# Kernel tuning notes

Hardware: AMD Instinct MI355X
Metric: run time of the kernel (lower is better)

The kernel has to match this reference:

```python
import jax, jax.numpy as jnp
import numpy as np

N_NODES = 100000
N_EDGES = 400000
F_IN = 128
HEADS = 4
C1 = 64   # conv1 out per head
C2 = 128  # conv2 out per head
G = 2048  # num graphs
FP = 2048
HID = 64
NEG_SLOPE = 0.2


def _gat_conv(x, edge_index, W, a_src, a_dst, b, heads, ch):
    """PyG-style GATConv with self-loops, concat=True."""
    n = x.shape[0]
    loops = jnp.arange(n, dtype=edge_index.dtype)
    src = jnp.concatenate([edge_index[0], loops])
    dst = jnp.concatenate([edge_index[1], loops])
    h = (x @ W).reshape(n, heads, ch)                      # [N,H,C]
    e_src = jnp.sum(h * a_src, axis=-1)                    # [N,H]
    e_dst = jnp.sum(h * a_dst, axis=-1)                    # [N,H]
    logits = jax.nn.leaky_relu(e_src[src] + e_dst[dst], NEG_SLOPE)  # [E,H]
    m = jax.ops.segment_max(logits, dst, num_segments=n)   # per-dst max
    p = jnp.exp(logits - m[dst])
    denom = jax.ops.segment_sum(p, dst, num_segments=n)
    alpha = p / denom[dst]                                 # [E,H]
    out = jax.ops.segment_sum(h[src] * alpha[:, :, None], dst, num_segments=n)
    return out.reshape(n, heads * ch) + b


def setup_inputs() -> dict:
    key = jax.random.key(0)
    ks = jax.random.split(key, 16)
    s = 0.05
    inp = {
        "x": jax.random.normal(ks[0], (N_NODES, F_IN), jnp.float32),
        "edge_index": jax.random.randint(ks[1], (2, N_EDGES), 0, N_NODES, jnp.int32),
        "batch": jnp.sort(jax.random.randint(ks[2], (N_NODES,), 0, G, jnp.int32)),
        "fp": jax.random.normal(ks[3], (G, FP), jnp.float32),
        "W1": jax.random.normal(ks[4], (F_IN, HEADS * C1), jnp.float32) * s,
        "a_src1": jax.random.normal(ks[5], (HEADS, C1), jnp.float32) * s,
        "a_dst1": jax.random.normal(ks[6], (HEADS, C1), jnp.float32) * s,
        "b1": jnp.zeros((HEADS * C1,), jnp.float32),
        "W2": jax.random.normal(ks[7], (HEADS * C1, HEADS * C2), jnp.float32) * s,
        "a_src2": jax.random.normal(ks[8], (HEADS, C2), jnp.float32) * s,
        "a_dst2": jax.random.normal(ks[9], (HEADS, C2), jnp.float32) * s,
        "b2": jnp.zeros((HEADS * C2,), jnp.float32),
        "Wfp": jax.random.normal(ks[10], (FP, HID), jnp.float32) * s,
        "bfp": jnp.zeros((HID,), jnp.float32),
        "Wfc1": jax.random.normal(ks[11], (HEADS * C2 + HID, HID), jnp.float32) * s,
        "bfc1": jnp.zeros((HID,), jnp.float32),
        "Wfc2": jax.random.normal(ks[12], (HID, 1), jnp.float32) * s,
        "bfc2": jnp.zeros((1,), jnp.float32),
    }
    return inp


def reference(x, edge_index, batch, fp, W1, a_src1, a_dst1, b1, W2, a_src2, a_dst2, b2,
              Wfp, bfp, Wfc1, bfc1, Wfc2, bfc2):
    h = _gat_conv(x, edge_index, W1, a_src1, a_dst1, b1, HEADS, C1)
    h = jax.nn.elu(h)
    h = _gat_conv(h, edge_index, W2, a_src2, a_dst2, b2, HEADS, C2)
    h = jax.nn.elu(h)
    # global mean pool over graphs
    sums = jax.ops.segment_sum(h, batch, num_segments=G)
    counts = jax.ops.segment_sum(jnp.ones((h.shape[0], 1), h.dtype), batch, num_segments=G)
    pooled = sums / jnp.maximum(counts, 1.0)               # [G, 512]
    fph = fp @ Wfp + bfp                                   # [G, 64]
    z = jnp.concatenate([pooled, fph], axis=1)             # [G, 576]
    z = jax.nn.relu(z @ Wfc1 + bfc1)
    # dropout is identity in eval mode
    return z @ Wfc2 + bfc2                                 # [G, 1]
```

## Files before the change

### kernel.cpp

```cpp
#include <hip/hip_runtime.h>
#include <math.h>

#define NEG_SLOPE 0.2f

typedef __attribute__((ext_vector_type(8))) short bf16x8;
typedef __attribute__((ext_vector_type(4))) float f32x4;
typedef __attribute__((ext_vector_type(2))) float f32x2;

__device__ __forceinline__ float b2f(short s) {
  return __uint_as_float(((unsigned int)(unsigned short)s) << 16);
}
__device__ __forceinline__ unsigned short f2b_rne(float f) {
  unsigned int u = __float_as_uint(f);
  u = (u + 0x7FFF + ((u >> 16) & 1)) >> 16;
  return (unsigned short)u;
}

__device__ __forceinline__ void fp8x8_to_f32(uint2 raw, float* f) {
  f32x2 a = __builtin_amdgcn_cvt_pk_f32_fp8((int)raw.x, false);
  f32x2 b = __builtin_amdgcn_cvt_pk_f32_fp8((int)raw.x, true);
  f32x2 c = __builtin_amdgcn_cvt_pk_f32_fp8((int)raw.y, false);
  f32x2 d = __builtin_amdgcn_cvt_pk_f32_fp8((int)raw.y, true);
  f[0] = a[0]; f[1] = a[1]; f[2] = b[0]; f[3] = b[1];
  f[4] = c[0]; f[5] = c[1]; f[6] = d[0]; f[7] = d[1];
}

__device__ __forceinline__ void gload16(const unsigned short* g, unsigned short* l) {
  __builtin_amdgcn_global_load_lds(
      (const __attribute__((address_space(1))) unsigned int*)g,
      (__attribute__((address_space(3))) unsigned int*)l, 16, 0, 0);
}

template<int N> __device__ __forceinline__ void vmwait() {
  asm volatile("s_waitcnt vmcnt(%0)" :: "n"(N) : "memory");
}

__device__ __forceinline__ unsigned int bsel(uint4 d, int s) {
  return ((d.x >> (8 * s)) & 0xffu) | (((d.y >> (8 * s)) & 0xffu) << 8)
       | (((d.z >> (8 * s)) & 0xffu) << 16) | (((d.w >> (8 * s)) & 0xffu) << 24);
}

__device__ __forceinline__ void tr_one(const float* __restrict__ W,
                                       unsigned short* __restrict__ WT,
                                       int K, int N, int idx)
{
  if (idx < K * N) {
    int k = idx / N, n = idx - k * N;
    WT[(size_t)n * K + k] = f2b_rne(W[idx]);
  }
}

__global__ __launch_bounds__(256) void prep_all(
    const float* __restrict__ x, unsigned short* __restrict__ xb, size_t nx, int B0,
    const float* __restrict__ fp, unsigned short* __restrict__ fpb, size_t nf, int B1,
    const float* __restrict__ W1, unsigned short* __restrict__ W1T,
    const float* __restrict__ W2, unsigned short* __restrict__ W2T,
    const float* __restrict__ Wfp, unsigned short* __restrict__ WfpT,
    const float* __restrict__ Wfc1, unsigned short* __restrict__ Wfc1T)
{
  int b = blockIdx.x;
  const int t = threadIdx.x;
  if (b < B0) {
    size_t i = (size_t)b * 256 + t;
    if (i < nx) xb[i] = f2b_rne(x[i]);
    return;
  }
  b -= B0;
  if (b < B1) {
    size_t i = (size_t)b * 256 + t;
    if (i < nf) fpb[i] = f2b_rne(fp[i]);
    return;
  }
  b -= B1;
  if (b < 128) { tr_one(W1, W1T, 128, 256, b * 256 + t); return; }
  b -= 128;
  if (b < 512) { tr_one(W2, W2T, 256, 512, b * 256 + t); return; }
  b -= 512;
  if (b < 512) { tr_one(Wfp, WfpT, 2048, 64, b * 256 + t); return; }
  b -= 512;
  tr_one(Wfc1, Wfc1T, 576, 64, b * 256 + t);
}

__global__ __launch_bounds__(256) void prep_e(
    const float* __restrict__ W1, const float* __restrict__ as1, const float* __restrict__ ad1,
    const float* __restrict__ W2, const float* __restrict__ as2, const float* __restrict__ ad2,
    unsigned short* __restrict__ BeT1, unsigned short* __restrict__ BeT2)
{
  const int b = blockIdx.x;
  const int k = threadIdx.x;
  if (b < 4) {
    if (k < 128) {
      float ss = 0.f, sd = 0.f;
      for (int c = 0; c < 64; ++c) {
        float w = W1[k * 256 + b * 64 + c];
        ss += w * as1[b * 64 + c];
        sd += w * ad1[b * 64 + c];
      }
      BeT1[b * 128 + k] = f2b_rne(ss);
      BeT1[(4 + b) * 128 + k] = f2b_rne(sd);
    }
  } else {
    const int h = b - 4;
    float ss = 0.f, sd = 0.f;
    for (int c = 0; c < 128; ++c) {
      float w = W2[k * 512 + h * 128 + c];
      ss += w * as2[h * 128 + c];
      sd += w * ad2[h * 128 + c];
    }
    BeT2[h * 256 + k] = f2b_rne(ss);
    BeT2[(4 + h) * 256 + k] = f2b_rne(sd);
  }
}

template<int KK>
__global__ __launch_bounds__(256) void gemm_mfma(
    const unsigned short* __restrict__ A, const unsigned short* __restrict__ BT,
    unsigned char* __restrict__ Cout, int M, int N,
    const unsigned short* __restrict__ BeT,
    float* __restrict__ es, float* __restrict__ ed, int nh)
{
  constexpr int NT = KK / 32;
  constexpr int LDE = KK + 8;
  __shared__ unsigned short As[4][128 * 32];
  __shared__ unsigned short Bs[4][128 * 32];
  __shared__ unsigned short Be[16 * LDE];
  const int tid  = threadIdx.x;
  const int wave = tid >> 6;
  const int lane = tid & 63;
  const int ln   = lane & 15;
  const int quad = lane >> 4;
  const int wr0  = (wave >> 1) * 64;
  const int wc0  = (wave & 1) * 64;

  const int nwg = gridDim.x;
  const int ncol = N >> 7;
  const int bid = blockIdx.x;
  const int qq = nwg >> 3, rr = nwg & 7;
  const int xc = bid & 7, io = bid >> 3;
  const int swz = (xc < rr ? xc * (qq + 1) : rr * (qq + 1) + (xc - rr) * qq) + io;
  const int bn = (swz % ncol) * 128;
  const int bm = (swz / ncol) * 128;
  const bool do_e = (bn == 0) && (wc0 == 0);

  if (bn == 0 && tid < KK) {
    const int rrw = tid / (KK / 8);
    const int ccl = (tid % (KK / 8)) * 8;
    bf16x8 v = *(const bf16x8*)(BeT + rrw * KK + ccl);
    *(bf16x8*)(&Be[rrw * LDE + ccl]) = v;
  }
  __syncthreads();

  const int srow = lane >> 2;
  const int cch  = lane & 3;
  const int rt0  = wave * 32 + srow;
  const int ksw  = ((cch ^ (srow & 3)) << 3);
  int ar0 = bm + rt0;      if (ar0 >= M) ar0 = M - 1;
  int ar1 = bm + rt0 + 16; if (ar1 >= M) ar1 = M - 1;
  const unsigned short* gA0 = A + (size_t)ar0 * KK + ksw;
  const unsigned short* gA1 = A + (size_t)ar1 * KK + ksw;
  const unsigned short* gB0 = BT + (size_t)(bn + rt0) * KK + ksw;
  const unsigned short* gB1 = BT + (size_t)(bn + rt0 + 16) * KK + ksw;

  auto stage = [&](int T) {
    const int b = T & 3;
    const int kk = T * 32;
    gload16(gA0 + kk, &As[b][(wave * 32) * 32]);
    gload16(gA1 + kk, &As[b][(wave * 32 + 16) * 32]);
    gload16(gB0 + kk, &Bs[b][(wave * 32) * 32]);
    gload16(gB1 + kk, &Bs[b][(wave * 32 + 16) * 32]);
  };

  f32x4 acc[4][4];
  f32x4 acc_e[4];
  const f32x4 z4 = {0.f, 0.f, 0.f, 0.f};
#pragma unroll
  for (int i = 0; i < 4; ++i) {
    acc_e[i] = z4;
#pragma unroll
    for (int j = 0; j < 4; ++j) acc[i][j] = z4;
  }

  stage(0); stage(1); stage(2);

#pragma unroll
  for (int t = 0; t < NT; ++t) {
    if (t + 3 < NT) stage(t + 3);
    if      (t < NT - 3) vmwait<12>();
    else if (t == NT - 3) vmwait<8>();
    else if (t == NT - 2) vmwait<4>();
    else                  vmwait<0>();
    __builtin_amdgcn_s_barrier();
    __builtin_amdgcn_sched_barrier(0);
    const int b = t & 3;
    bf16x8 af[4], bfv[4];
#pragma unroll
    for (int i = 0; i < 4; ++i) {
      const int row = wr0 + i * 16 + ln;
      af[i] = *(const bf16x8*)(&As[b][row * 32 + ((quad ^ (ln & 3)) << 3)]);
    }
#pragma unroll
    for (int j = 0; j < 4; ++j) {
      const int row = wc0 + j * 16 + ln;
      bfv[j] = *(const bf16x8*)(&Bs[b][row * 32 + ((quad ^ (ln & 3)) << 3)]);
    }
#pragma unroll
    for (int i = 0; i < 4; ++i)
#pragma unroll
      for (int j = 0; j < 4; ++j)
        acc[i][j] = __builtin_amdgcn_mfma_f32_16x16x32_bf16(af[i], bfv[j], acc[i][j], 0, 0, 0);
    if (do_e) {
      bf16x8 bfe = *(const bf16x8*)(&Be[ln * LDE + t * 32 + quad * 8]);
#pragma unroll
      for (int i = 0; i < 4; ++i)
        acc_e[i] = __builtin_amdgcn_mfma_f32_16x16x32_bf16(af[i], bfe, acc_e[i], 0, 0, 0);
    }
    __builtin_amdgcn_sched_barrier(0);
    __builtin_amdgcn_s_barrier();
  }
  __syncthreads();

  unsigned int* Cb = (unsigned int*)As;
  const int cbase = (wc0 >> 2) + ln;
#pragma unroll
  for (int i = 0; i < 4; ++i) {
#pragma unroll
    for (int r = 0; r < 4; ++r) {
      int rowl = wr0 + i * 16 + quad * 4 + r;
      int p = __builtin_amdgcn_cvt_pk_fp8_f32(acc[i][0][r], acc[i][1][r], 0, false);
      p     = __builtin_amdgcn_cvt_pk_fp8_f32(acc[i][2][r], acc[i][3][r], p, true);
      Cb[rowl * 36 + cbase] = (unsigned int)p;
    }
  }
  if (do_e) {
#pragma unroll
    for (int i = 0; i < 4; ++i) {
#pragma unroll
      for (int r = 0; r < 4; ++r) {
        int row = bm + wr0 + i * 16 + quad * 4 + r;
        if (row < M && ln < 8) {
          float* dst = (ln < 4) ? es : ed;
          dst[(size_t)row * nh + (ln & 3)] = acc_e[i][r];
        }
      }
    }
  }
  __syncthreads();

  {
    const int rT = tid >> 1;
    const int hT = tid & 1;
    const unsigned int* cp = &Cb[rT * 36 + 16 * hT];
    uint4 d0 = *(const uint4*)(cp + 0);
    uint4 d1 = *(const uint4*)(cp + 4);
    uint4 d2 = *(const uint4*)(cp + 8);
    uint4 d3 = *(const uint4*)(cp + 12);
    int grow = bm + rT;
    if (grow < M) {
      unsigned char* gp = Cout + (size_t)grow * N + bn + 64 * hT;
      uint4 o;
      o.x = bsel(d0, 0); o.y = bsel(d1, 0); o.z = bsel(d2, 0); o.w = bsel(d3, 0);
      *(uint4*)(gp + 0) = o;
      o.x = bsel(d0, 1); o.y = bsel(d1, 1); o.z = bsel(d2, 1); o.w = bsel(d3, 1);
      *(uint4*)(gp + 16) = o;
      o.x = bsel(d0, 2); o.y = bsel(d1, 2); o.z = bsel(d2, 2); o.w = bsel(d3, 2);
      *(uint4*)(gp + 32) = o;
      o.x = bsel(d0, 3); o.y = bsel(d1, 3); o.z = bsel(d2, 3); o.w = bsel(d3, 3);
      *(uint4*)(gp + 48) = o;
    }
  }
}

__global__ __launch_bounds__(256) void gemm_mfma_n64(
    const unsigned short* __restrict__ A, int lda,
    const unsigned short* __restrict__ BT, int ldb,
    float* __restrict__ Cp, int M, int kchunk)
{
  const int LDT = 72;
  __shared__ unsigned short As[128 * 72];
  __shared__ unsigned short Bs[64 * 72];
  const int tid  = threadIdx.x;
  const int wave = tid >> 6;
  const int lane = tid & 63;
  const int ln   = lane & 15;
  const int quad = lane >> 4;
  const int ks   = blockIdx.x;
  const int bm   = blockIdx.y * 128;
  const int k_beg = ks * kchunk;
  const int k_end = k_beg + kchunk;
  const int arow = tid >> 1;
  const int akb  = (tid & 1) * 32;
  const int brow = tid >> 2;
  const int bkb  = (tid & 3) * 16;

  f32x4 acc[2][4];
  const f32x4 z4 = {0.f, 0.f, 0.f, 0.f};
#pragma unroll
  for (int i = 0; i < 2; ++i)
#pragma unroll
    for (int j = 0; j < 4; ++j) acc[i][j] = z4;

  for (int k0 = k_beg; k0 < k_end; k0 += 64) {
    const unsigned short* ap = A + (size_t)(bm + arow) * lda + k0 + akb;
#pragma unroll
    for (int q = 0; q < 4; ++q)
      *(bf16x8*)(&As[arow * LDT + akb + q * 8]) = *(const bf16x8*)(ap + q * 8);
    const unsigned short* bp = BT + (size_t)brow * ldb + k0 + bkb;
#pragma unroll
    for (int q = 0; q < 2; ++q)
      *(bf16x8*)(&Bs[brow * LDT + bkb + q * 8]) = *(const bf16x8*)(bp + q * 8);
    __syncthreads();
#pragma unroll
    for (int kk = 0; kk < 2; ++kk) {
      bf16x8 af[2], bfv[4];
#pragma unroll
      for (int i = 0; i < 2; ++i)
        af[i] = *(const bf16x8*)(&As[(wave * 32 + i * 16 + ln) * LDT + kk * 32 + quad * 8]);
#pragma unroll
      for (int j = 0; j < 4; ++j)
        bfv[j] = *(const bf16x8*)(&Bs[(j * 16 + ln) * LDT + kk * 32 + quad * 8]);
#pragma unroll
      for (int i = 0; i < 2; ++i)
#pragma unroll
        for (int j = 0; j < 4; ++j)
          acc[i][j] = __builtin_amdgcn_mfma_f32_16x16x32_bf16(af[i], bfv[j], acc[i][j], 0, 0, 0);
    }
    __syncthreads();
  }
#pragma unroll
  for (int i = 0; i < 2; ++i)
#pragma unroll
    for (int r = 0; r < 4; ++r) {
      int row = bm + wave * 32 + i * 16 + quad * 4 + r;
#pragma unroll
      for (int j = 0; j < 4; ++j)
        Cp[((size_t)ks * M + row) * 64 + j * 16 + ln] = acc[i][j][r];
    }
}

__global__ void fp_finish(const float* __restrict__ Cp, int ksplit, int M,
                          const float* __restrict__ bfp,
                          unsigned short* __restrict__ zb)
{
  const int g = blockIdx.x;
  const int j = threadIdx.x;
  float s = bfp[j];
  for (int ks = 0; ks < ksplit; ++ks) s += Cp[((size_t)ks * M + g) * 64 + j];
  zb[(size_t)g * 576 + 512 + j] = f2b_rne(s);
}

__global__ void mlp_finish(const float* __restrict__ Cp, int ksplit, int M,
                           const float* __restrict__ bfc1,
                           const float* __restrict__ Wfc2, const float* __restrict__ bfc2,
                           float* __restrict__ out)
{
  const int g = blockIdx.x;
  const int j = threadIdx.x;
  float s = bfc1[j];
  for (int ks = 0; ks < ksplit; ++ks) s += Cp[((size_t)ks * M + g) * 64 + j];
  s = s > 0.f ? s : 0.f;
  float term = s * Wfc2[j];
  for (int off = 32; off; off >>= 1) term += __shfl_down(term, off, 64);
  if (j == 0) out[g] = term + bfc2[0];
}

__global__ void count_all(const int* __restrict__ ei, int E, int* __restrict__ deg,
                          const int* __restrict__ batch, int NN, int* __restrict__ gcnt,
                          int BE)
{
  int b = blockIdx.x;
  int t = threadIdx.x;
  if (b < BE) {
    int e = b * 256 + t;
    if (e < E) atomicAdd(&deg[ei[E + e]], 1);
  } else {
    int i = (b - BE) * 256 + t;
    if (i < NN) atomicAdd(&gcnt[batch[i]], 1);
  }
}

__global__ void fill_csr(const int* __restrict__ ei, int E, int* __restrict__ cursor,
                         const int* __restrict__ rowptr, int* __restrict__ csr_src)
{
  int e = blockIdx.x * 256 + threadIdx.x;
  if (e < E) {
    int d = ei[E + e];
    int pos = atomicAdd(&cursor[d], 1);
    csr_src[rowptr[d] + pos] = ei[e];
  }
}

__device__ void scan_p1_body(const int* __restrict__ vals, int n, int* __restrict__ bsum,
                             int bb)
{
  __shared__ int red[256];
  int base = bb * 1024;
  int t = threadIdx.x;
  int s = 0;
#pragma unroll
  for (int i = 0; i < 4; ++i) {
    int idx = base + i * 256 + t;
    if (idx < n) s += vals[idx];
  }
  red[t] = s;
  __syncthreads();
  for (int off = 128; off; off >>= 1) {
    if (t < off) red[t] += red[t + off];
    __syncthreads();
  }
  if (t == 0) bsum[bb] = red[0];
}

__global__ void scan2_p1(const int* __restrict__ vA, int nA, int* __restrict__ bsA, int nbA,
                         const int* __restrict__ vB, int nB, int* __restrict__ bsB)
{
  int b = blockIdx.x;
  if (b < nbA) scan_p1_body(vA, nA, bsA, b);
  else         scan_p1_body(vB, nB, bsB, b - nbA);
}

__device__ void scan_p2_body(const int* __restrict__ bsum, int* __restrict__ bpre,
                             int nb, int* __restrict__ rowptr, int n)
{
  __shared__ int tmp[128];
  int t = threadIdx.x;
  int v = (t < nb) ? bsum[t] : 0;
  tmp[t] = v;
  __syncthreads();
  for (int off = 1; off < 128; off <<= 1) {
    int add = (t >= off) ? tmp[t - off] : 0;
    __syncthreads();
    tmp[t] += add;
    __syncthreads();
  }
  if (t < nb) bpre[t] = tmp[t] - v;
  if (t == 127) rowptr[n] = tmp[127];
}

__global__ void scan2_p2(const int* __restrict__ bsA, int* __restrict__ bpA, int nbA,
                         int* __restrict__ rpA, int nA,
                         const int* __restrict__ bsB, int* __restrict__ bpB, int nbB,
                         int* __restrict__ rpB, int nB)
{
  if (blockIdx.x == 0) scan_p2_body(bsA, bpA, nbA, rpA, nA);
  else                 scan_p2_body(bsB, bpB, nbB, rpB, nB);
}

__device__ void scan_p3_body(const int* __restrict__ vals, const int* __restrict__ bpre,
                             int n, int* __restrict__ rowptr, int bb)
{
  __shared__ int tmp[256];
  int t = threadIdx.x;
  int base = bb * 1024 + t * 4;
  int v[4]; int s = 0;
#pragma unroll
  for (int i = 0; i < 4; ++i) {
    int idx = base + i;
    v[i] = (idx < n) ? vals[idx] : 0;
    s += v[i];
  }
  tmp[t] = s;
  __syncthreads();
  for (int off = 1; off < 256; off <<= 1) {
    int add = (t >= off) ? tmp[t - off] : 0;
    __syncthreads();
    tmp[t] += add;
    __syncthreads();
  }
  int run = bpre[bb] + tmp[t] - s;
#pragma unroll
  for (int i = 0; i < 4; ++i) {
    int idx = base + i;
    if (idx < n) rowptr[idx] = run;
    run += v[i];
  }
}

__global__ void scan2_p3(const int* __restrict__ vA, const int* __restrict__ bpA, int nA,
                         int* __restrict__ rpA, int nbA,
                         const int* __restrict__ vB, const int* __restrict__ bpB, int nB,
                         int* __restrict__ rpB)
{
  int b = blockIdx.x;
  if (b < nbA) scan_p3_body(vA, bpA, nA, rpA, b);
  else         scan_p3_body(vB, bpB, nB, rpB, b - nbA);
}

__global__ void alpha_kernel(const float* __restrict__ es, const float* __restrict__ ed,
                             const int* __restrict__ rowptr, const int* __restrict__ csr_src,
                             float* __restrict__ w_csr, float* __restrict__ wself,
                             float* __restrict__ dinv, int N, int nh)
{
  int idx = blockIdx.x * 256 + threadIdx.x;
  if (idx >= N * nh) return;
  const int dst = idx / nh;
  const int h = idx - dst * nh;
  const float edh = ed[(size_t)dst * nh + h];
  const int beg = rowptr[dst], end = rowptr[dst + 1];
  float sum = 0.f;
  for (int e = beg; e < end; ++e) {
    int s = csr_src[e];
    float l = es[(size_t)s * nh + h] + edh;
    l = l >= 0.f ? l : NEG_SLOPE * l;
    float w = expf(l);
    w_csr[(size_t)e * nh + h] = w;
    sum += w;
  }
  float ls = es[(size_t)dst * nh + h] + edh;
  ls = ls >= 0.f ? ls : NEG_SLOPE * ls;
  float wsl = expf(ls);
  sum += wsl;
  wself[(size_t)dst * nh + h] = wsl;
  dinv[(size_t)dst * nh + h] = 1.0f / sum;
}

__global__ __launch_bounds__(256) void aggregate_b(
    const unsigned char* __restrict__ h,
    const float* __restrict__ w_csr, const float* __restrict__ wself,
    const float* __restrict__ dinv,
    const int* __restrict__ rowptr, const int* __restrict__ csr_src,
    const float* __restrict__ bias, unsigned short* __restrict__ out,
    int N, int nh, int C)
{
  const int HC = nh * C;
  const int CH8 = HC >> 3;
  const int dpb = 256 / CH8;
  const int grp = threadIdx.x / CH8;
  const int lane = threadIdx.x - grp * CH8;
  const int dst = blockIdx.x * dpb + grp;
  if (dst >= N) return;
  const int ch = lane << 3;
  const int head = ch / C;
  const int beg = rowptr[dst], end = rowptr[dst + 1];
  float acc[8] = {0.f, 0.f, 0.f, 0.f, 0.f, 0.f, 0.f, 0.f};
  float hv[8];
  int e = beg;
  for (; e + 1 < end; e += 2) {
    int s0 = csr_src[e], s1 = csr_src[e + 1];
    float a0 = w_csr[(size_t)e * nh + head];
    float a1 = w_csr[(size_t)(e + 1) * nh + head];
    uint2 r0 = *(const uint2*)(h + (size_t)s0 * HC + ch);
    uint2 r1 = *(const uint2*)(h + (size_t)s1 * HC + ch);
    fp8x8_to_f32(r0, hv);
#pragma unroll
    for (int r = 0; r < 8; ++r) acc[r] = fmaf(a0, hv[r], acc[r]);
    fp8x8_to_f32(r1, hv);
#pragma unroll
    for (int r = 0; r < 8; ++r) acc[r] = fmaf(a1, hv[r], acc[r]);
  }
  if (e < end) {
    int s0 = csr_src[e];
    float a0 = w_csr[(size_t)e * nh + head];
    uint2 r0 = *(const uint2*)(h + (size_t)s0 * HC + ch);
    fp8x8_to_f32(r0, hv);
#pragma unroll
    for (int r = 0; r < 8; ++r) acc[r] = fmaf(a0, hv[r], acc[r]);
  }
  {
    float a = wself[(size_t)dst * nh + head];
    uint2 r0 = *(const uint2*)(h + (size_t)dst * HC + ch);
    fp8x8_to_f32(r0, hv);
#pragma unroll
    for (int r = 0; r < 8; ++r) acc[r] = fmaf(a, hv[r], acc[r]);
  }
  const float di = dinv[(size_t)dst * nh + head];
  bf16x8 o;
#pragma unroll
  for (int r = 0; r < 8; ++r) {
    float v = acc[r] * di + bias[ch + r];
    v = v > 0.f ? v : (expf(v) - 1.0f);
    o[r] = (short)f2b_rne(v);
  }
  *(bf16x8*)(out + (size_t)dst * HC + ch) = o;
}

__global__ __launch_bounds__(256) void agg_pool(
    const unsigned char* __restrict__ h,
    const float* __restrict__ w_csr, const float* __restrict__ wself,
    const float* __restrict__ dinv,
    const int* __restrict__ rowptr, const int* __restrict__ csr_src,
    const float* __restrict__ bias, const int* __restrict__ grp,
    unsigned short* __restrict__ zb)
{
  const int g = blockIdx.x;
  const int wave = threadIdx.x >> 6;
  const int lane = threadIdx.x & 63;
  const int ch = lane << 3;
  const int head = lane >> 4;
  const int gbeg = grp[g], gend = grp[g + 1];
  float bch[8];
#pragma unroll
  for (int r = 0; r < 8; ++r) bch[r] = bias[ch + r];
  float pool[8] = {0.f, 0.f, 0.f, 0.f, 0.f, 0.f, 0.f, 0.f};
  float hv[8];

  for (int node = gbeg + wave; node < gend; node += 4) {
    const int beg = rowptr[node], end = rowptr[node + 1];
    float acc[8] = {0.f, 0.f, 0.f, 0.f, 0.f, 0.f, 0.f, 0.f};
    int e = beg;
    for (; e + 1 < end; e += 2) {
      int s0 = csr_src[e], s1 = csr_src[e + 1];
      float a0 = w_csr[(size_t)e * 4 + head];
      float a1 = w_csr[(size_t)(e + 1) * 4 + head];
      uint2 r0 = *(const uint2*)(h + (size_t)s0 * 512 + ch);
      uint2 r1 = *(const uint2*)(h + (size_t)s1 * 512 + ch);
      fp8x8_to_f32(r0, hv);
#pragma unroll
      for (int r = 0; r < 8; ++r) acc[r] = fmaf(a0, hv[r], acc[r]);
      fp8x8_to_f32(r1, hv);
#pragma unroll
      for (int r = 0; r < 8; ++r) acc[r] = fmaf(a1, hv[r], acc[r]);
    }
    if (e < end) {
      int s0 = csr_src[e];
      float a0 = w_csr[(size_t)e * 4 + head];
      uint2 r0 = *(const uint2*)(h + (size_t)s0 * 512 + ch);
      fp8x8_to_f32(r0, hv);
#pragma unroll
      for (int r = 0; r < 8; ++r) acc[r] = fmaf(a0, hv[r], acc[r]);
    }
    {
      float a = wself[(size_t)node * 4 + head];
      uint2 r0 = *(const uint2*)(h + (size_t)node * 512 + ch);
      fp8x8_to_f32(r0, hv);
#pragma unroll
      for (int r = 0; r < 8; ++r) acc[r] = fmaf(a, hv[r], acc[r]);
    }
    const float di = dinv[(size_t)node * 4 + head];
#pragma unroll
    for (int r = 0; r < 8; ++r) {
      float v = acc[r] * di + bch[r];
      v = v > 0.f ? v : (expf(v) - 1.0f);
      pool[r] += v;
    }
  }

  __shared__ float red[4][512];
#pragma unroll
  for (int r = 0; r < 8; ++r) red[wave][ch + r] = pool[r];
  __syncthreads();
  const float inv = 1.0f / (float)max(gend - gbeg, 1);
#pragma unroll
  for (int k = 0; k < 2; ++k) {
    int c = threadIdx.x + k * 256;
    float s = (red[0][c] + red[1][c]) + (red[2][c] + red[3][c]);
    zb[(size_t)g * 576 + c] = f2b_rne(s * inv);
  }
}

extern "C" void kernel_launch(void* const* d_in, const int* in_sizes, int n_in,
                              void* d_out, int out_size, void* d_ws, size_t ws_size,
                              hipStream_t stream)
{
  const float* x      = (const float*)d_in[0];
  const int*   ei     = (const int*)d_in[1];
  const int*   batch  = (const int*)d_in[2];
  const float* fp     = (const float*)d_in[3];
  const float* W1     = (const float*)d_in[4];
  const float* a_src1 = (const float*)d_in[5];
  const float* a_dst1 = (const float*)d_in[6];
  const float* b1     = (const float*)d_in[7];
  const float* W2     = (const float*)d_in[8];
  const float* a_src2 = (const float*)d_in[9];
  const float* a_dst2 = (const float*)d_in[10];
  const float* b2     = (const float*)d_in[11];
  const float* Wfp    = (const float*)d_in[12];
  const float* bfp    = (const float*)d_in[13];
  const float* Wfc1   = (const float*)d_in[14];
  const float* bfc1   = (const float*)d_in[15];
  const float* Wfc2   = (const float*)d_in[16];
  const float* bfc2   = (const float*)d_in[17];
  float* out = (float*)d_out;

  const int NN = in_sizes[0] / 128;
  const int E  = in_sizes[1] / 2;
  const int G  = in_sizes[3] / 2048;
  const int FIN = 128, H = 4, C1 = 64, C2 = 128;
  const int HC1 = H * C1;
  const int HC2 = H * C2;
  const int KFP = in_sizes[3] / G;
  const int KZ  = HC2 + 64;
  const int KS_FP = 16;
  const int KS_Z  = 9;

  char* base = (char*)d_ws;
  size_t off = 0;
  auto alloc = [&](size_t bytes) {
    char* p = base + off; off += (bytes + 255) & ~(size_t)255; return p;
  };
  size_t xb_sz  = ((size_t)NN * FIN * 2 + 255) & ~(size_t)255;
  size_t h1b_sz = (size_t)NN * HC1;
  size_t h2b_sz = (size_t)NN * HC2;
  size_t rA = xb_sz + h1b_sz; if (h2b_sz > rA) rA = h2b_sz;
  char* RA = alloc(rA);
  unsigned short* xb  = (unsigned short*)RA;
  unsigned char*  h1b = (unsigned char*)(RA + xb_sz);
  unsigned char*  h2b = (unsigned char*)RA;
  size_t fpb_sz  = ((size_t)G * KFP * 2 + 255) & ~(size_t)255;
  size_t cpfp_sz = (size_t)KS_FP * G * 64 * 4;
  size_t agg1_sz = (size_t)NN * HC1 * 2;
  size_t rB = fpb_sz + cpfp_sz; if (agg1_sz > rB) rB = agg1_sz;
  char* RB = alloc(rB);
  unsigned short* fpb   = (unsigned short*)RB;
  float*          Cp_fp = (float*)(RB + fpb_sz);
  unsigned short* agg1b = (unsigned short*)RB;
  float* w1     = (float*)alloc((size_t)E * H * 4);
  float* wself1 = (float*)alloc((size_t)NN * H * 4);
  float* es1    = (float*)alloc((size_t)NN * H * 4);
  float* ed1    = (float*)alloc((size_t)NN * H * 4);
  float* dinv1  = (float*)alloc((size_t)NN * H * 4);
  float* w2 = w1, *wself2 = wself1, *es2 = es1, *ed2 = ed1, *dinv2 = dinv1;
  unsigned short* zb    = (unsigned short*)alloc((size_t)G * KZ * 2);
  float*          Cp_z  = (float*)alloc((size_t)KS_Z * G * 64 * 4);
  unsigned short* W1T   = (unsigned short*)alloc((size_t)HC1 * FIN * 2);
  unsigned short* W2T   = (unsigned short*)alloc((size_t)HC2 * HC1 * 2);
  unsigned short* WfpT  = (unsigned short*)alloc((size_t)64 * KFP * 2);
  unsigned short* Wfc1T = (unsigned short*)alloc((size_t)64 * KZ * 2);
  unsigned short* BeT1  = (unsigned short*)alloc((size_t)8 * 128 * 2);
  unsigned short* BeT2  = (unsigned short*)alloc((size_t)8 * 256 * 2);
  int* iarena   = (int*)alloc(((size_t)2 * NN + G) * 4);
  int* deg      = iarena;
  int* cursor   = iarena + NN;
  int* gcnt     = iarena + 2 * NN;
  int* rowptr_n = (int*)alloc(((size_t)NN + 1) * 4);
  int* rowptr_g = (int*)alloc(((size_t)G + 1) * 4);
  int* csr_src  = (int*)alloc((size_t)E * 4);
  int* bsumA    = (int*)alloc(128 * 4);
  int* bpreA    = (int*)alloc(128 * 4);
  int* bsumB    = (int*)alloc(128 * 4);
  int* bpreB    = (int*)alloc(128 * 4);

  const size_t nx = (size_t)NN * FIN;
  const size_t nf = (size_t)G * KFP;
  const int B0 = (int)((nx + 255) / 256);
  const int B1 = (int)((nf + 255) / 256);
  {
    int nb = B0 + B1 + 128 + 512 + 512 + 144;
    prep_all<<<nb, 256, 0, stream>>>(x, xb, nx, B0, fp, fpb, nf, B1,
                                     W1, W1T, W2, W2T, Wfp, WfpT, Wfc1, Wfc1T);
  }
  prep_e<<<8, 256, 0, stream>>>(W1, a_src1, a_dst1, W2, a_src2, a_dst2, BeT1, BeT2);

  {
    dim3 gg(KS_FP, G / 128);
    gemm_mfma_n64<<<gg, 256, 0, stream>>>(fpb, KFP, WfpT, KFP, Cp_fp, G, KFP / KS_FP);
    fp_finish<<<G, 64, 0, stream>>>(Cp_fp, KS_FP, G, bfp, zb);
  }

  hipMemsetAsync(iarena, 0, sizeof(int) * ((size_t)2 * NN + G), stream);
  {
    int BE = (E + 255) / 256;
    int BN = (NN + 255) / 256;
    count_all<<<BE + BN, 256, 0, stream>>>(ei, E, deg, batch, NN, gcnt, BE);
  }
  {
    int nbA = (NN + 1023) / 1024;
    int nbB = (G + 1023) / 1024;
    scan2_p1<<<nbA + nbB, 256, 0, stream>>>(deg, NN, bsumA, nbA, gcnt, G, bsumB);
    scan2_p2<<<2, 128, 0, stream>>>(bsumA, bpreA, nbA, rowptr_n, NN,
                                    bsumB, bpreB, nbB, rowptr_g, G);
    scan2_p3<<<nbA + nbB, 256, 0, stream>>>(deg, bpreA, NN, rowptr_n, nbA,
                                            gcnt, bpreB, G, rowptr_g);
  }
  fill_csr<<<(E + 255) / 256, 256, 0, stream>>>(ei, E, cursor, rowptr_n, csr_src);

  {
    const int nrow = (NN + 127) / 128;
    gemm_mfma<128><<<nrow * (HC1 / 128), 256, 0, stream>>>(
        xb, W1T, h1b, NN, HC1, BeT1, es1, ed1, H);
  }
  alpha_kernel<<<(NN * H + 255) / 256, 256, 0, stream>>>(es1, ed1, rowptr_n, csr_src,
                                                         w1, wself1, dinv1, NN, H);
  aggregate_b<<<(NN + 7) / 8, 256, 0, stream>>>(h1b, w1, wself1, dinv1, rowptr_n, csr_src,
                                                b1, agg1b, NN, H, C1);

  {
    const int nrow = (NN + 127) / 128;
    gemm_mfma<256><<<nrow * (HC2 / 128), 256, 0, stream>>>(
        agg1b, W2T, h2b, NN, HC2, BeT2, es2, ed2, H);
  }
  alpha_kernel<<<(NN * H + 255) / 256, 256, 0, stream>>>(es2, ed2, rowptr_n, csr_src,
                                                         w2, wself2, dinv2, NN, H);
  agg_pool<<<G, 256, 0, stream>>>(h2b, w2, wself2, dinv2, rowptr_n, csr_src,
                                  b2, rowptr_g, zb);

  {
    dim3 gg(KS_Z, G / 128);
    gemm_mfma_n64<<<gg, 256, 0, stream>>>(zb, KZ, Wfc1T, KZ, Cp_z, G, KZ / KS_Z);
    mlp_finish<<<G, 64, 0, stream>>>(Cp_z, KS_Z, G, bfc1, Wfc2, bfc2, out);
  }
}
```

Measured before the change: 451.6 us.

## Fuse attention weight computation into aggregation kernels, drop alpha_kernel

Removes the separate alpha_kernel launches for both GAT layers. The aggregation kernels now compute leaky-relu/exp edge weights and the softmax denominator inline from es/ed, instead of writing and rereading per-edge weight arrays. This removes two launches and the edge-weight memory traffic. In exchange, each lane of a head group recomputes the same exp per edge, and the max-subtraction is still omitted, as it was before.

Measured after the change: 462.0 us. 1.02x slower.

```diff
diff --git a/kernel.cpp b/kernel.cpp
--- a/kernel.cpp
+++ b/kernel.cpp
@@ -38,6 +38,11 @@
 __device__ __forceinline__ unsigned int bsel(uint4 d, int s) {
   return ((d.x >> (8 * s)) & 0xffu) | (((d.y >> (8 * s)) & 0xffu) << 8)
        | (((d.z >> (8 * s)) & 0xffu) << 16) | (((d.w >> (8 * s)) & 0xffu) << 24);
+}
+
+__device__ __forceinline__ float lrelu_exp(float l) {
+  l = l >= 0.f ? l : NEG_SLOPE * l;
+  return expf(l);
 }
 
 __device__ __forceinline__ void tr_one(const float* __restrict__ W,
@@ -485,38 +490,9 @@
   else         scan_p3_body(vB, bpB, nB, rpB, b - nbA);
 }
 
-__global__ void alpha_kernel(const float* __restrict__ es, const float* __restrict__ ed,
-                             const int* __restrict__ rowptr, const int* __restrict__ csr_src,
-                             float* __restrict__ w_csr, float* __restrict__ wself,
-                             float* __restrict__ dinv, int N, int nh)
-{
-  int idx = blockIdx.x * 256 + threadIdx.x;
-  if (idx >= N * nh) return;
-  const int dst = idx / nh;
-  const int h = idx - dst * nh;
-  const float edh = ed[(size_t)dst * nh + h];
-  const int beg = rowptr[dst], end = rowptr[dst + 1];
-  float sum = 0.f;
-  for (int e = beg; e < end; ++e) {
-    int s = csr_src[e];
-    float l = es[(size_t)s * nh + h] + edh;
-    l = l >= 0.f ? l : NEG_SLOPE * l;
-    float w = expf(l);
-    w_csr[(size_t)e * nh + h] = w;
-    sum += w;
-  }
-  float ls = es[(size_t)dst * nh + h] + edh;
-  ls = ls >= 0.f ? ls : NEG_SLOPE * ls;
-  float wsl = expf(ls);
-  sum += wsl;
-  wself[(size_t)dst * nh + h] = wsl;
-  dinv[(size_t)dst * nh + h] = 1.0f / sum;
-}
-
 __global__ __launch_bounds__(256) void aggregate_b(
     const unsigned char* __restrict__ h,
-    const float* __restrict__ w_csr, const float* __restrict__ wself,
-    const float* __restrict__ dinv,
+    const float* __restrict__ es, const float* __restrict__ ed,
     const int* __restrict__ rowptr, const int* __restrict__ csr_src,
     const float* __restrict__ bias, unsigned short* __restrict__ out,
     int N, int nh, int C)
@@ -530,39 +506,48 @@
   if (dst >= N) return;
   const int ch = lane << 3;
   const int head = ch / C;
+  const float edh = ed[(size_t)dst * nh + head];
   const int beg = rowptr[dst], end = rowptr[dst + 1];
   float acc[8] = {0.f, 0.f, 0.f, 0.f, 0.f, 0.f, 0.f, 0.f};
   float hv[8];
+  float sum = 0.f;
   int e = beg;
   for (; e + 1 < end; e += 2) {
     int s0 = csr_src[e], s1 = csr_src[e + 1];
-    float a0 = w_csr[(size_t)e * nh + head];
-    float a1 = w_csr[(size_t)(e + 1) * nh + head];
+    float l0 = es[(size_t)s0 * nh + head] + edh;
+    float l1 = es[(size_t)s1 * nh + head] + edh;
     uint2 r0 = *(const uint2*)(h + (size_t)s0 * HC + ch);
     uint2 r1 = *(const uint2*)(h + (size_t)s1 * HC + ch);
+    float a0 = lrelu_exp(l0);
+    float a1 = lrelu_exp(l1);
     fp8x8_to_f32(r0, hv);
 #pragma unroll
     for (int r = 0; r < 8; ++r) acc[r] = fmaf(a0, hv[r], acc[r]);
     fp8x8_to_f32(r1, hv);
 #pragma unroll
     for (int r = 0; r < 8; ++r) acc[r] = fmaf(a1, hv[r], acc[r]);
+    sum += a0; sum += a1;
   }
   if (e < end) {
     int s0 = csr_src[e];
-    float a0 = w_csr[(size_t)e * nh + head];
+    float l0 = es[(size_t)s0 * nh + head] + edh;
     uint2 r0 = *(const uint2*)(h + (size_t)s0 * HC + ch);
+    float a0 = lrelu_exp(l0);
     fp8x8_to_f32(r0, hv);
 #pragma unroll
     for (int r = 0; r < 8; ++r) acc[r] = fmaf(a0, hv[r], acc[r]);
-  }
-  {
-    float a = wself[(size_t)dst * nh + head];
+    sum += a0;
+  }
+  {
+    float ls = es[(size_t)dst * nh + head] + edh;
+    float a = lrelu_exp(ls);
     uint2 r0 = *(const uint2*)(h + (size_t)dst * HC + ch);
     fp8x8_to_f32(r0, hv);
 #pragma unroll
     for (int r = 0; r < 8; ++r) acc[r] = fmaf(a, hv[r], acc[r]);
-  }
-  const float di = dinv[(size_t)dst * nh + head];
+    sum += a;
+  }
+  const float di = 1.0f / sum;
   bf16x8 o;
 #pragma unroll
   for (int r = 0; r < 8; ++r) {
@@ -575,8 +560,7 @@
 
 __global__ __launch_bounds__(256) void agg_pool(
     const unsigned char* __restrict__ h,
-    const float* __restrict__ w_csr, const float* __restrict__ wself,
-    const float* __restrict__ dinv,
+    const float* __restrict__ es, const float* __restrict__ ed,
     const int* __restrict__ rowptr, const int* __restrict__ csr_src,
     const float* __restrict__ bias, const int* __restrict__ grp,
     unsigned short* __restrict__ zb)
@@ -595,37 +579,46 @@
 
   for (int node = gbeg + wave; node < gend; node += 4) {
     const int beg = rowptr[node], end = rowptr[node + 1];
+    const float edh = ed[(size_t)node * 4 + head];
     float acc[8] = {0.f, 0.f, 0.f, 0.f, 0.f, 0.f, 0.f, 0.f};
+    float sum = 0.f;
     int e = beg;
     for (; e + 1 < end; e += 2) {
       int s0 = csr_src[e], s1 = csr_src[e + 1];
-      float a0 = w_csr[(size_t)e * 4 + head];
-      float a1 = w_csr[(size_t)(e + 1) * 4 + head];
+      float l0 = es[(size_t)s0 * 4 + head] + edh;
+      float l1 = es[(size_t)s1 * 4 + head] + edh;
       uint2 r0 = *(const uint2*)(h + (size_t)s0 * 512 + ch);
       uint2 r1 = *(const uint2*)(h + (size_t)s1 * 512 + ch);
+      float a0 = lrelu_exp(l0);
+      float a1 = lrelu_exp(l1);
       fp8x8_to_f32(r0, hv);
 #pragma unroll
       for (int r = 0; r < 8; ++r) acc[r] = fmaf(a0, hv[r], acc[r]);
       fp8x8_to_f32(r1, hv);
 #pragma unroll
       for (int r = 0; r < 8; ++r) acc[r] = fmaf(a1, hv[r], acc[r]);
+      sum += a0; sum += a1;
     }
     if (e < end) {
       int s0 = csr_src[e];
-      float a0 = w_csr[(size_t)e * 4 + head];
+      float l0 = es[(size_t)s0 * 4 + head] + edh;
       uint2 r0 = *(const uint2*)(h + (size_t)s0 * 512 + ch);
+      float a0 = lrelu_exp(l0);
       fp8x8_to_f32(r0, hv);
 #pragma unroll
       for (int r = 0; r < 8; ++r) acc[r] = fmaf(a0, hv[r], acc[r]);
+      sum += a0;
     }
     {
-      float a = wself[(size_t)node * 4 + head];
+      float ls = es[(size_t)node * 4 + head] + edh;
+      float a = lrelu_exp(ls);
       uint2 r0 = *(const uint2*)(h + (size_t)node * 512 + ch);
       fp8x8_to_f32(r0, hv);
 #pragma unroll
       for (int r = 0; r < 8; ++r) acc[r] = fmaf(a, hv[r], acc[r]);
-    }
-    const float di = dinv[(size_t)node * 4 + head];
+      sum += a;
+    }
+    const float di = 1.0f / sum;
 #pragma unroll
     for (int r = 0; r < 8; ++r) {
       float v = acc[r] * di + bch[r];
@@ -703,12 +696,9 @@
   unsigned short* fpb   = (unsigned short*)RB;
   float*          Cp_fp = (float*)(RB + fpb_sz);
   unsigned short* agg1b = (unsigned short*)RB;
-  float* w1     = (float*)alloc((size_t)E * H * 4);
-  float* wself1 = (float*)alloc((size_t)NN * H * 4);
   float* es1    = (float*)alloc((size_t)NN * H * 4);
   float* ed1    = (float*)alloc((size_t)NN * H * 4);
-  float* dinv1  = (float*)alloc((size_t)NN * H * 4);
-  float* w2 = w1, *wself2 = wself1, *es2 = es1, *ed2 = ed1, *dinv2 = dinv1;
+  float* es2 = es1, *ed2 = ed1;
   unsigned short* zb    = (unsigned short*)alloc((size_t)G * KZ * 2);
   float*          Cp_z  = (float*)alloc((size_t)KS_Z * G * 64 * 4);
   unsigned short* W1T   = (unsigned short*)alloc((size_t)HC1 * FIN * 2);
@@ -768,9 +758,7 @@
     gemm_mfma<128><<<nrow * (HC1 / 128), 256, 0, stream>>>(
         xb, W1T, h1b, NN, HC1, BeT1, es1, ed1, H);
   }
-  alpha_kernel<<<(NN * H + 255) / 256, 256, 0, stream>>>(es1, ed1, rowptr_n, csr_src,
-                                                         w1, wself1, dinv1, NN, H);
-  aggregate_b<<<(NN + 7) / 8, 256, 0, stream>>>(h1b, w1, wself1, dinv1, rowptr_n, csr_src,
+  aggregate_b<<<(NN + 7) / 8, 256, 0, stream>>>(h1b, es1, ed1, rowptr_n, csr_src,
                                                 b1, agg1b, NN, H, C1);
 
   {
@@ -778,9 +766,7 @@
     gemm_mfma<256><<<nrow * (HC2 / 128), 256, 0, stream>>>(
         agg1b, W2T, h2b, NN, HC2, BeT2, es2, ed2, H);
   }
-  alpha_kernel<<<(NN * H + 255) / 256, 256, 0, stream>>>(es2, ed2, rowptr_n, csr_src,
-                                                         w2, wself2, dinv2, NN, H);
-  agg_pool<<<G, 256, 0, stream>>>(h2b, w2, wself2, dinv2, rowptr_n, csr_src,
+  agg_pool<<<G, 256, 0, stream>>>(h2b, es2, ed2, rowptr_n, csr_src,
                                   b2, rowptr_g, zb);
 
   {
```
